# Optimization experiments

Hardware: AMD Instinct MI355X
Metric: run time of the kernel (lower is better)

## Reference

```python
import jax, jax.numpy as jnp
import numpy as np

N_NODES = 100000
N_EDGES = 3200000
D_IN = 256
D_OUT = 256


def setup_inputs() -> dict:
    key = jax.random.key(0)
    k1, k2, k3, k4, k5 = jax.random.split(key, 5)
    x = jax.random.normal(k1, (N_NODES, D_IN), dtype=jnp.float32)
    W = jax.random.normal(k2, (D_OUT, D_IN), dtype=jnp.float32) * (1.0 / np.sqrt(D_IN))
    edge_val = jax.random.uniform(k3, (N_EDGES,), dtype=jnp.float32)
    edge_row = jax.random.randint(k4, (N_EDGES,), 0, N_NODES, dtype=jnp.int32)
    edge_col = jax.random.randint(k5, (N_EDGES,), 0, N_NODES, dtype=jnp.int32)
    return {"x": x, "W": W, "edge_val": edge_val, "edge_row": edge_row, "edge_col": edge_col}


def reference(x, W, edge_val, edge_row, edge_col):
    # Linear (no bias): [N, D_in] @ [D_in, D_out] -> [N, D_out]
    h = x @ W.T
    # SpMM: out[r] = sum_e val[e] * h[col[e]] for edges with row[e] == r
    msgs = h[edge_col] * edge_val[:, None]          # [E, D_out] gather + scale
    out = jax.ops.segment_sum(msgs, edge_row, num_segments=N_NODES)  # scatter-add
    return out
```

## Files before the change

kernel.cpp:

```cpp
#include <hip/hip_runtime.h>
#include <hip/hip_bf16.h>

typedef float  f32x4 __attribute__((ext_vector_type(4)));
typedef short  s16x8 __attribute__((ext_vector_type(8)));
typedef unsigned short u16x8 __attribute__((ext_vector_type(8)));

#define N_NODES 100000
#define N_EDGES 3200000
#define DD 256

#define ROWS_PER_BKT 128
#define NBKT 782
#define BKT_CAP 4608
#define ACHUNK 3072
#define NABLK 1042
#define EDGES_PER_THREAD 12

#define BM 64
#define BN 256
#define BK 64
#define LDA 72
#define GEMM_BLOCKS 1563
#define NPAD (GEMM_BLOCKS * BM)
#define QSTRIDE 272

#define K1_LDS (4*NBKT*4 + 256*4 + ACHUNK*8 + ACHUNK*4)

__device__ __forceinline__ ushort f2bf(float f) {
    union { __hip_bfloat16 b; ushort u; } cv;
    cv.b = __float2bfloat16(f);
    return cv.u;
}

__global__ __launch_bounds__(256) void wconv_kernel(const float* __restrict__ w, ushort* __restrict__ wb)
{
    int gid = blockIdx.x * 256 + threadIdx.x;
    float4 a = ((const float4*)w)[gid * 2];
    float4 b = ((const float4*)w)[gid * 2 + 1];
    u16x8 o = { f2bf(a.x), f2bf(a.y), f2bf(a.z), f2bf(a.w),
                f2bf(b.x), f2bf(b.y), f2bf(b.z), f2bf(b.w) };
    ((u16x8*)wb)[gid] = o;
}

__global__ __launch_bounds__(256) void k1_kernel(
    const float* __restrict__ x, const ushort* __restrict__ wb,
    unsigned char* __restrict__ h8, float* __restrict__ hscale,
    const int* __restrict__ erow, const int* __restrict__ ecol,
    const float* __restrict__ eval, int* __restrict__ gcur,
    int2* __restrict__ pairsA)
{
    extern __shared__ char smem[];
    const int tid = threadIdx.x;

    if (blockIdx.x < GEMM_BLOCKS) {
        ushort (*xs)[LDA]  = (ushort(*)[LDA])smem;
        ushort (*wsx)[LDA] = (ushort(*)[LDA])(smem + BM * LDA * 2);
        const int lane = tid & 63;
        const int wq   = tid >> 6;
        const int bm   = blockIdx.x * BM;
        const int l15 = lane & 15;
        const int lhi = lane >> 4;
        f32x4 acc[4][4] = {};

        for (int k0 = 0; k0 < DD; k0 += BK) {
            #pragma unroll
            for (int it = 0; it < 4; ++it) {
                int f = (it * 256 + tid) * 4;
                int r = f >> 6, c = f & 63;
                float4 v = make_float4(0.f, 0.f, 0.f, 0.f);
                if (bm + r < N_NODES) v = *(const float4*)(x + (size_t)(bm + r) * DD + k0 + c);
                *(ushort4*)&xs[r][c] = make_ushort4(f2bf(v.x), f2bf(v.y), f2bf(v.z), f2bf(v.w));
            }
            #pragma unroll
            for (int it = 0; it < 8; ++it) {
                int f = (it * 256 + tid) * 8;
                int r = f >> 6, c = f & 63;
                *(uint4*)&wsx[r][c] = *(const uint4*)(wb + (size_t)r * DD + k0 + c);
            }
            __syncthreads();
            #pragma unroll
            for (int kk = 0; kk < 2; ++kk) {
                const int koff = kk * 32 + lhi * 8;
                s16x8 a[4], b[4];
                #pragma unroll
                for (int m = 0; m < 4; ++m)
                    a[m] = *(const s16x8*)&xs[m * 16 + l15][koff];
                #pragma unroll
                for (int n = 0; n < 4; ++n)
                    b[n] = *(const s16x8*)&wsx[wq * 64 + n * 16 + l15][koff];
                #pragma unroll
                for (int m = 0; m < 4; ++m)
                    #pragma unroll
                    for (int n = 0; n < 4; ++n)
                        acc[m][n] = __builtin_amdgcn_mfma_f32_16x16x32_bf16(a[m], b[n], acc[m][n], 0, 0, 0);
            }
            __syncthreads();
        }

        float* wmax = (float*)smem;
        unsigned char* i8buf = (unsigned char*)(smem + 1024);

        float pmax[4][4];
        #pragma unroll
        for (int m = 0; m < 4; ++m)
            #pragma unroll
            for (int r = 0; r < 4; ++r)
                pmax[m][r] = fmaxf(fmaxf(fabsf(acc[m][0][r]), fabsf(acc[m][1][r])),
                                   fmaxf(fabsf(acc[m][2][r]), fabsf(acc[m][3][r])));
        #pragma unroll
        for (int s = 1; s < 16; s <<= 1)
            #pragma unroll
            for (int m = 0; m < 4; ++m)
                #pragma unroll
                for (int r = 0; r < 4; ++r)
                    pmax[m][r] = fmaxf(pmax[m][r], __shfl_xor(pmax[m][r], s));
        if (l15 == 0) {
            #pragma unroll
            for (int m = 0; m < 4; ++m)
                #pragma unroll
                for (int r = 0; r < 4; ++r)
                    wmax[(m * 16 + lhi * 4 + r) * 4 + wq] = pmax[m][r];
        }
        __syncthreads();
        #pragma unroll
        for (int m = 0; m < 4; ++m)
            #pragma unroll
            for (int r = 0; r < 4; ++r) {
                const int R = m * 16 + lhi * 4 + r;
                f32x4 wv = *(const f32x4*)&wmax[R * 4];
                float rmax = fmaxf(fmaxf(fmaxf(wv[0], wv[1]), fmaxf(wv[2], wv[3])), 1e-30f);
                const float sc = 127.0f / rmax;
                #pragma unroll
                for (int n = 0; n < 4; ++n) {
                    int q = (int)rintf(acc[m][n][r] * sc);
                    i8buf[R * QSTRIDE + wq * 64 + n * 16 + l15] = (unsigned char)q;
                }
                if (wq == 0 && l15 == 0)
                    hscale[bm + R] = rmax * (1.0f / 127.0f);
            }
        __syncthreads();
        #pragma unroll
        for (int it = 0; it < 4; ++it) {
            int idx = it * 256 + tid;
            int R = idx >> 4, w = idx & 15;
            *(uint4*)(h8 + (size_t)bm * 256 + (size_t)idx * 16) =
                *(const uint4*)&i8buf[R * QSTRIDE + w * 16];
        }
        return;
    }

    int*  hist   = (int*)smem;
    int*  sbase  = hist  + NBKT;
    int*  scur   = sbase + NBKT;
    int*  rbase  = scur  + NBKT;
    int*  gsum   = rbase + NBKT;
    int2* staged = (int2*)(gsum + 256);
    int*  gdst   = (int*)(staged + ACHUNK);

    for (int i = tid; i < NBKT; i += 256) hist[i] = 0;
    __syncthreads();
    const int base = (blockIdx.x - GEMM_BLOCKS) * ACHUNK;
    int pk[EDGES_PER_THREAD]; float vv[EDGES_PER_THREAD]; int bk[EDGES_PER_THREAD];
    #pragma unroll
    for (int k = 0; k < EDGES_PER_THREAD; ++k) {
        int i = base + k * 256 + tid;
        bk[k] = -1;
        if (i < N_EDGES) {
            int r = erow[i];
            bk[k] = r >> 7;
            pk[k] = ecol[i] | ((r & 127) << 17);
            vv[k] = eval[i];
            atomicAdd(&hist[bk[k]], 1);
        }
    }
    __syncthreads();
    int gs = 0, lv[4];
    #pragma unroll
    for (int j = 0; j < 4; ++j) {
        int b = tid * 4 + j;
        lv[j] = (b < NBKT) ? hist[b] : 0;
        gs += lv[j];
    }
    gsum[tid] = gs;
    __syncthreads();
    for (int s = 1; s < 256; s <<= 1) {
        int t = (tid >= s) ? gsum[tid - s] : 0;
        __syncthreads();
        gsum[tid] += t;
        __syncthreads();
    }
    int run = gsum[tid] - gs;
    #pragma unroll
    for (int j = 0; j < 4; ++j) {
        int b = tid * 4 + j;
        if (b < NBKT) { sbase[b] = run; scur[b] = run; }
        run += lv[j];
    }
    __syncthreads();
    for (int b = tid; b < NBKT; b += 256) {
        int c = hist[b];
        if (c) rbase[b] = atomicAdd(&gcur[b], c);
    }
    __syncthreads();
    #pragma unroll
    for (int k = 0; k < EDGES_PER_THREAD; ++k) {
        if (bk[k] >= 0) {
            int lo = atomicAdd(&scur[bk[k]], 1);
            staged[lo] = make_int2(pk[k], __float_as_int(vv[k]));
            gdst[lo] = bk[k] * BKT_CAP + rbase[bk[k]] + (lo - sbase[bk[k]]);
        }
    }
    __syncthreads();
    const int cnt = min(ACHUNK, N_EDGES - base);
    for (int t = tid; t < cnt; t += 256)
        pairsA[gdst[t]] = staged[t];
}

__global__ __launch_bounds__(256) void passB_kernel(
    const int2* __restrict__ pairsA, const int* __restrict__ gcur,
    int2* __restrict__ pairsB, int2* __restrict__ row_se)
{
    __shared__ int hist[ROWS_PER_BKT];
    __shared__ int lds[ROWS_PER_BKT];
    __shared__ int cur[ROWS_PER_BKT];
    const int tid = threadIdx.x;
    const int b = blockIdx.x;
    const int cnt = gcur[b];
    const int base = b * BKT_CAP;
    if (tid < ROWS_PER_BKT) hist[tid] = 0;
    __syncthreads();
    for (int i = tid; i < cnt; i += 256)
        atomicAdd(&hist[(pairsA[base + i].x >> 17) & 127], 1);
    __syncthreads();
    int v = (tid < ROWS_PER_BKT) ? hist[tid] : 0;
    if (tid < ROWS_PER_BKT) lds[tid] = v;
    __syncthreads();
    for (int st = 1; st < ROWS_PER_BKT; st <<= 1) {
        int t = (tid >= st && tid < ROWS_PER_BKT) ? lds[tid - st] : 0;
        __syncthreads();
        if (tid < ROWS_PER_BKT) lds[tid] += t;
        __syncthreads();
    }
    if (tid < ROWS_PER_BKT) {
        int excl = lds[tid] - v;
        int r = b * ROWS_PER_BKT + tid;
        if (r < N_NODES) row_se[r] = make_int2(base + excl, base + excl + v);
        cur[tid] = base + excl;
    }
    __syncthreads();
    for (int i = tid; i < cnt; i += 256) {
        int2 p = pairsA[base + i];
        int rl = (p.x >> 17) & 127;
        int d = atomicAdd(&cur[rl], 1);
        pairsB[d] = make_int2(p.x & 0x1FFFF, p.y);
    }
}

__global__ __launch_bounds__(256) void spmm_kernel(
    const unsigned char* __restrict__ h8, const float* __restrict__ hscale,
    const int2* __restrict__ pairs, const int2* __restrict__ row_se,
    float* __restrict__ out)
{
    const int wid  = blockIdx.x * 4 + (threadIdx.x >> 6);
    const int lane = threadIdx.x & 63;
    if (wid >= N_NODES) return;
    const int2 se = row_se[wid];
    const int s = __builtin_amdgcn_readfirstlane(se.x);
    const int e = __builtin_amdgcn_readfirstlane(se.y);
    const int loff = lane * 4;
    float ax = 0.f, ay = 0.f, az = 0.f, aw = 0.f;

    int j = s;
    for (; j + 8 <= e; j += 8) {
        const int4* p4 = (const int4*)(pairs + j);
        int4 q0 = p4[0], q1 = p4[1], q2 = p4[2], q3 = p4[3];
        int   c[8] = { q0.x, q0.z, q1.x, q1.z, q2.x, q2.z, q3.x, q3.z };
        float v[8] = { __int_as_float(q0.y), __int_as_float(q0.w),
                       __int_as_float(q1.y), __int_as_float(q1.w),
                       __int_as_float(q2.y), __int_as_float(q2.w),
                       __int_as_float(q3.y), __int_as_float(q3.w) };
        float vs[8];
        #pragma unroll
        for (int t = 0; t < 8; ++t) vs[t] = v[t] * hscale[c[t]];
        unsigned hv[8];
        #pragma unroll
        for (int t = 0; t < 8; ++t)
            hv[t] = *(const unsigned*)(h8 + (size_t)c[t] * DD + loff);
        #pragma unroll
        for (int t = 0; t < 8; ++t) {
            ax += vs[t] * (float)((int)(hv[t] << 24) >> 24);
            ay += vs[t] * (float)((int)(hv[t] << 16) >> 24);
            az += vs[t] * (float)((int)(hv[t] <<  8) >> 24);
            aw += vs[t] * (float)((int)hv[t] >> 24);
        }
    }
    for (; j < e; ++j) {
        int2 p = pairs[j];
        const float vs = __int_as_float(p.y) * hscale[p.x];
        const unsigned hv = *(const unsigned*)(h8 + (size_t)p.x * DD + loff);
        ax += vs * (float)((int)(hv << 24) >> 24);
        ay += vs * (float)((int)(hv << 16) >> 24);
        az += vs * (float)((int)(hv <<  8) >> 24);
        aw += vs * (float)((int)hv >> 24);
    }
    f32x4 o = { ax, ay, az, aw };
    __builtin_nontemporal_store(o, (f32x4*)(out + (size_t)wid * DD + loff));
}

extern "C" void kernel_launch(void* const* d_in, const int* in_sizes, int n_in,
                              void* d_out, int out_size, void* d_ws, size_t ws_size,
                              hipStream_t stream)
{
    const float* x        = (const float*)d_in[0];
    const float* W        = (const float*)d_in[1];
    const float* edge_val = (const float*)d_in[2];
    const int*   edge_row = (const int*)d_in[3];
    const int*   edge_col = (const int*)d_in[4];
    float* out = (float*)d_out;

    char* ws = (char*)d_ws;
    size_t off = 0;
    auto alloc = [&](size_t bytes) {
        void* p = ws + off;
        off = (off + bytes + 255) & ~(size_t)255;
        return p;
    };
    unsigned char* h8     = (unsigned char*)alloc((size_t)NPAD * DD);
    float*         hscale = (float*)        alloc((size_t)NPAD * sizeof(float));
    int2*          pairsA = (int2*)alloc((size_t)NBKT * BKT_CAP * sizeof(int2));
    int2*          pairsB = (int2*)alloc((size_t)NBKT * BKT_CAP * sizeof(int2));
    ushort*        wb     = (ushort*)alloc((size_t)DD * DD * sizeof(ushort));
    int*           gcur   = (int*)alloc((size_t)NBKT * sizeof(int));
    int2*          row_se = (int2*)alloc((size_t)N_NODES * sizeof(int2));
    (void)ws_size;

    (void)hipMemsetAsync(gcur, 0, (size_t)NBKT * sizeof(int), stream);

    wconv_kernel<<<DD * DD / 8 / 256, 256, 0, stream>>>(W, wb);

    k1_kernel<<<GEMM_BLOCKS + NABLK, 256, K1_LDS, stream>>>(
        x, wb, h8, hscale, edge_row, edge_col, edge_val, gcur, pairsA);

    passB_kernel<<<NBKT, 256, 0, stream>>>(pairsA, gcur, pairsB, row_se);

    int spmm_blocks = (N_NODES + 3) / 4;
    spmm_kernel<<<spmm_blocks, 256, 0, stream>>>(h8, hscale, pairsB, row_se, out);
}
```

Baseline: 240.3 us.

## Split fused GEMM/bucketing kernel into separate GEMM and pass-A kernels

The fused kernel that ran the bf16 GEMM with int8 quantization and the edge-bucketing pass as disjoint block ranges is split into two kernels launched one after the other. Each kernel now uses static shared memory sized to its own needs, so GEMM blocks no longer reserve the large bucketing LDS footprint and can run at higher occupancy. The cost is that the GEMM and bucketing work no longer overlap on the GPU, plus one extra launch. A reciprocal intrinsic also replaces the division when computing the quantization scale.

```diff
diff --git a/kernel.cpp b/kernel.cpp
--- a/kernel.cpp
+++ b/kernel.cpp
@@ -24,8 +24,6 @@
 #define NPAD (GEMM_BLOCKS * BM)
 #define QSTRIDE 272
 
-#define K1_LDS (4*NBKT*4 + 256*4 + ACHUNK*8 + ACHUNK*4)
-
 __device__ __forceinline__ ushort f2bf(float f) {
     union { __hip_bfloat16 b; ushort u; } cv;
     cv.b = __float2bfloat16(f);
@@ -42,124 +40,123 @@
     ((u16x8*)wb)[gid] = o;
 }
 
-__global__ __launch_bounds__(256) void k1_kernel(
+__global__ __launch_bounds__(256) void gemm_q_kernel(
     const float* __restrict__ x, const ushort* __restrict__ wb,
-    unsigned char* __restrict__ h8, float* __restrict__ hscale,
+    unsigned char* __restrict__ h8, float* __restrict__ hscale)
+{
+    __shared__ char smem[BM * LDA * 2 + BN * LDA * 2];
+    ushort (*xs)[LDA]  = (ushort(*)[LDA])smem;
+    ushort (*wsx)[LDA] = (ushort(*)[LDA])(smem + BM * LDA * 2);
+    const int tid  = threadIdx.x;
+    const int lane = tid & 63;
+    const int wq   = tid >> 6;
+    const int bm   = blockIdx.x * BM;
+    const int l15 = lane & 15;
+    const int lhi = lane >> 4;
+    f32x4 acc[4][4] = {};
+
+    for (int k0 = 0; k0 < DD; k0 += BK) {
+        #pragma unroll
+        for (int it = 0; it < 4; ++it) {
+            int f = (it * 256 + tid) * 4;
+            int r = f >> 6, c = f & 63;
+            float4 v = make_float4(0.f, 0.f, 0.f, 0.f);
+            if (bm + r < N_NODES) v = *(const float4*)(x + (size_t)(bm + r) * DD + k0 + c);
+            *(ushort4*)&xs[r][c] = make_ushort4(f2bf(v.x), f2bf(v.y), f2bf(v.z), f2bf(v.w));
+        }
+        #pragma unroll
+        for (int it = 0; it < 8; ++it) {
+            int f = (it * 256 + tid) * 8;
+            int r = f >> 6, c = f & 63;
+            *(uint4*)&wsx[r][c] = *(const uint4*)(wb + (size_t)r * DD + k0 + c);
+        }
+        __syncthreads();
+        #pragma unroll
+        for (int kk = 0; kk < 2; ++kk) {
+            const int koff = kk * 32 + lhi * 8;
+            s16x8 a[4], b[4];
+            #pragma unroll
+            for (int m = 0; m < 4; ++m)
+                a[m] = *(const s16x8*)&xs[m * 16 + l15][koff];
+            #pragma unroll
+            for (int n = 0; n < 4; ++n)
+                b[n] = *(const s16x8*)&wsx[wq * 64 + n * 16 + l15][koff];
+            #pragma unroll
+            for (int m = 0; m < 4; ++m)
+                #pragma unroll
+                for (int n = 0; n < 4; ++n)
+                    acc[m][n] = __builtin_amdgcn_mfma_f32_16x16x32_bf16(a[m], b[n], acc[m][n], 0, 0, 0);
+        }
+        __syncthreads();
+    }
+
+    float* wmax = (float*)smem;
+    unsigned char* i8buf = (unsigned char*)(smem + 1024);
+
+    float pmax[4][4];
+    #pragma unroll
+    for (int m = 0; m < 4; ++m)
+        #pragma unroll
+        for (int r = 0; r < 4; ++r)
+            pmax[m][r] = fmaxf(fmaxf(fabsf(acc[m][0][r]), fabsf(acc[m][1][r])),
+                               fmaxf(fabsf(acc[m][2][r]), fabsf(acc[m][3][r])));
+    #pragma unroll
+    for (int s = 1; s < 16; s <<= 1)
+        #pragma unroll
+        for (int m = 0; m < 4; ++m)
+            #pragma unroll
+            for (int r = 0; r < 4; ++r)
+                pmax[m][r] = fmaxf(pmax[m][r], __shfl_xor(pmax[m][r], s));
+    if (l15 == 0) {
+        #pragma unroll
+        for (int m = 0; m < 4; ++m)
+            #pragma unroll
+            for (int r = 0; r < 4; ++r)
+                wmax[(m * 16 + lhi * 4 + r) * 4 + wq] = pmax[m][r];
+    }
+    __syncthreads();
+    #pragma unroll
+    for (int m = 0; m < 4; ++m)
+        #pragma unroll
+        for (int r = 0; r < 4; ++r) {
+            const int R = m * 16 + lhi * 4 + r;
+            f32x4 wv = *(const f32x4*)&wmax[R * 4];
+            float rmax = fmaxf(fmaxf(fmaxf(wv[0], wv[1]), fmaxf(wv[2], wv[3])), 1e-30f);
+            const float sc = 127.0f * __builtin_amdgcn_rcpf(rmax);
+            #pragma unroll
+            for (int n = 0; n < 4; ++n) {
+                int q = (int)rintf(acc[m][n][r] * sc);
+                i8buf[R * QSTRIDE + wq * 64 + n * 16 + l15] = (unsigned char)q;
+            }
+            if (wq == 0 && l15 == 0)
+                hscale[bm + R] = rmax * (1.0f / 127.0f);
+        }
+    __syncthreads();
+    #pragma unroll
+    for (int it = 0; it < 4; ++it) {
+        int idx = it * 256 + tid;
+        int R = idx >> 4, w = idx & 15;
+        *(uint4*)(h8 + (size_t)bm * 256 + (size_t)idx * 16) =
+            *(const uint4*)&i8buf[R * QSTRIDE + w * 16];
+    }
+}
+
+__global__ __launch_bounds__(256) void passA_kernel(
     const int* __restrict__ erow, const int* __restrict__ ecol,
     const float* __restrict__ eval, int* __restrict__ gcur,
     int2* __restrict__ pairsA)
 {
-    extern __shared__ char smem[];
+    __shared__ int hist[NBKT];
+    __shared__ int sbase[NBKT];
+    __shared__ int scur[NBKT];
+    __shared__ int rbase[NBKT];
+    __shared__ int gsum[256];
+    __shared__ int2 staged[ACHUNK];
+    __shared__ int gdst[ACHUNK];
     const int tid = threadIdx.x;
-
-    if (blockIdx.x < GEMM_BLOCKS) {
-        ushort (*xs)[LDA]  = (ushort(*)[LDA])smem;
-        ushort (*wsx)[LDA] = (ushort(*)[LDA])(smem + BM * LDA * 2);
-        const int lane = tid & 63;
-        const int wq   = tid >> 6;
-        const int bm   = blockIdx.x * BM;
-        const int l15 = lane & 15;
-        const int lhi = lane >> 4;
-        f32x4 acc[4][4] = {};
-
-        for (int k0 = 0; k0 < DD; k0 += BK) {
-            #pragma unroll
-            for (int it = 0; it < 4; ++it) {
-                int f = (it * 256 + tid) * 4;
-                int r = f >> 6, c = f & 63;
-                float4 v = make_float4(0.f, 0.f, 0.f, 0.f);
-                if (bm + r < N_NODES) v = *(const float4*)(x + (size_t)(bm + r) * DD + k0 + c);
-                *(ushort4*)&xs[r][c] = make_ushort4(f2bf(v.x), f2bf(v.y), f2bf(v.z), f2bf(v.w));
-            }
-            #pragma unroll
-            for (int it = 0; it < 8; ++it) {
-                int f = (it * 256 + tid) * 8;
-                int r = f >> 6, c = f & 63;
-                *(uint4*)&wsx[r][c] = *(const uint4*)(wb + (size_t)r * DD + k0 + c);
-            }
-            __syncthreads();
-            #pragma unroll
-            for (int kk = 0; kk < 2; ++kk) {
-                const int koff = kk * 32 + lhi * 8;
-                s16x8 a[4], b[4];
-                #pragma unroll
-                for (int m = 0; m < 4; ++m)
-                    a[m] = *(const s16x8*)&xs[m * 16 + l15][koff];
-                #pragma unroll
-                for (int n = 0; n < 4; ++n)
-                    b[n] = *(const s16x8*)&wsx[wq * 64 + n * 16 + l15][koff];
-                #pragma unroll
-                for (int m = 0; m < 4; ++m)
-                    #pragma unroll
-                    for (int n = 0; n < 4; ++n)
-                        acc[m][n] = __builtin_amdgcn_mfma_f32_16x16x32_bf16(a[m], b[n], acc[m][n], 0, 0, 0);
-            }
-            __syncthreads();
-        }
-
-        float* wmax = (float*)smem;
-        unsigned char* i8buf = (unsigned char*)(smem + 1024);
-
-        float pmax[4][4];
-        #pragma unroll
-        for (int m = 0; m < 4; ++m)
-            #pragma unroll
-            for (int r = 0; r < 4; ++r)
-                pmax[m][r] = fmaxf(fmaxf(fabsf(acc[m][0][r]), fabsf(acc[m][1][r])),
-                                   fmaxf(fabsf(acc[m][2][r]), fabsf(acc[m][3][r])));
-        #pragma unroll
-        for (int s = 1; s < 16; s <<= 1)
-            #pragma unroll
-            for (int m = 0; m < 4; ++m)
-                #pragma unroll
-                for (int r = 0; r < 4; ++r)
-                    pmax[m][r] = fmaxf(pmax[m][r], __shfl_xor(pmax[m][r], s));
-        if (l15 == 0) {
-            #pragma unroll
-            for (int m = 0; m < 4; ++m)
-                #pragma unroll
-                for (int r = 0; r < 4; ++r)
-                    wmax[(m * 16 + lhi * 4 + r) * 4 + wq] = pmax[m][r];
-        }
-        __syncthreads();
-        #pragma unroll
-        for (int m = 0; m < 4; ++m)
-            #pragma unroll
-            for (int r = 0; r < 4; ++r) {
-                const int R = m * 16 + lhi * 4 + r;
-                f32x4 wv = *(const f32x4*)&wmax[R * 4];
-                float rmax = fmaxf(fmaxf(fmaxf(wv[0], wv[1]), fmaxf(wv[2], wv[3])), 1e-30f);
-                const float sc = 127.0f / rmax;
-                #pragma unroll
-                for (int n = 0; n < 4; ++n) {
-                    int q = (int)rintf(acc[m][n][r] * sc);
-                    i8buf[R * QSTRIDE + wq * 64 + n * 16 + l15] = (unsigned char)q;
-                }
-                if (wq == 0 && l15 == 0)
-                    hscale[bm + R] = rmax * (1.0f / 127.0f);
-            }
-        __syncthreads();
-        #pragma unroll
-        for (int it = 0; it < 4; ++it) {
-            int idx = it * 256 + tid;
-            int R = idx >> 4, w = idx & 15;
-            *(uint4*)(h8 + (size_t)bm * 256 + (size_t)idx * 16) =
-                *(const uint4*)&i8buf[R * QSTRIDE + w * 16];
-        }
-        return;
-    }
-
-    int*  hist   = (int*)smem;
-    int*  sbase  = hist  + NBKT;
-    int*  scur   = sbase + NBKT;
-    int*  rbase  = scur  + NBKT;
-    int*  gsum   = rbase + NBKT;
-    int2* staged = (int2*)(gsum + 256);
-    int*  gdst   = (int*)(staged + ACHUNK);
-
     for (int i = tid; i < NBKT; i += 256) hist[i] = 0;
     __syncthreads();
-    const int base = (blockIdx.x - GEMM_BLOCKS) * ACHUNK;
+    const int base = blockIdx.x * ACHUNK;
     int pk[EDGES_PER_THREAD]; float vv[EDGES_PER_THREAD]; int bk[EDGES_PER_THREAD];
     #pragma unroll
     for (int k = 0; k < EDGES_PER_THREAD; ++k) {
@@ -338,8 +335,9 @@
 
     wconv_kernel<<<DD * DD / 8 / 256, 256, 0, stream>>>(W, wb);
 
-    k1_kernel<<<GEMM_BLOCKS + NABLK, 256, K1_LDS, stream>>>(
-        x, wb, h8, hscale, edge_row, edge_col, edge_val, gcur, pairsA);
+    gemm_q_kernel<<<GEMM_BLOCKS, 256, 0, stream>>>(x, wb, h8, hscale);
+
+    passA_kernel<<<NABLK, 256, 0, stream>>>(edge_row, edge_col, edge_val, gcur, pairsA);
 
     passB_kernel<<<NBKT, 256, 0, stream>>>(pairsA, gcur, pairsB, row_se);
 
```

After: 263.5 us. +9.6%, slower.
